# Optimization experiments

Hardware: AMD Instinct MI355X
Metric: run time of the kernel (lower is better)

## Reference

```python
import jax, jax.numpy as jnp
import numpy as np

B, S, E, H = 2, 2048, 1024, 16
D = E // H  # head_dim = 64


def setup_inputs() -> dict:
    key = jax.random.key(0)
    ks = jax.random.split(key, 14)
    inp = {
        "query": jax.random.normal(ks[0], (B, S, E), jnp.float32),
        "key": jax.random.normal(ks[1], (B, S, E), jnp.float32),
        "value": jax.random.normal(ks[2], (B, S, E), jnp.float32),
        "adj": jax.random.normal(ks[3], (S, S), jnp.float32),
        "mask": jax.random.randint(ks[4], (B, 1, S, S), 0, 2, jnp.int32),
    }
    sc = 1.0 / np.sqrt(E)
    inp["Wq"] = jax.random.normal(ks[5], (E, E), jnp.float32) * sc
    inp["bq"] = jax.random.normal(ks[6], (E,), jnp.float32) * sc
    inp["Wk"] = jax.random.normal(ks[7], (E, E), jnp.float32) * sc
    inp["bk"] = jax.random.normal(ks[8], (E,), jnp.float32) * sc
    inp["Wv"] = jax.random.normal(ks[9], (E, E), jnp.float32) * sc
    inp["bv"] = jax.random.normal(ks[10], (E,), jnp.float32) * sc
    inp["Wo"] = jax.random.normal(ks[11], (E, E), jnp.float32) * sc
    inp["bo"] = jax.random.normal(ks[12], (E,), jnp.float32) * sc
    return inp


def reference(query, key, value, adj, mask, Wq, bq, Wk, bk, Wv, bv, Wo, bo):
    b, s, _ = query.shape
    # projections, split into heads: [B,S,E] -> [B,H,S,D]
    def heads(x, W, bias):
        y = jnp.einsum("bse,ef->bsf", x, W.T) + bias
        return y.reshape(b, s, H, D).transpose(0, 2, 1, 3)

    Q = heads(query, Wq, bq)
    K = heads(key, Wk, bk)
    V = heads(value, Wv, bv)

    # scores: [B,H,S,S], scaled by sqrt(head_dim), plus adjacency bias
    scores = jnp.einsum("bhqd,bhkd->bhqk", Q, K) / jnp.sqrt(jnp.float32(D))
    scores = scores + adj[None, None, :, :]
    scores = jnp.where(mask == 0, jnp.float32(-jnp.inf), scores)

    weights = jax.nn.softmax(scores, axis=-1)
    out = jnp.einsum("bhqk,bhkd->bhqd", weights, V)
    out = out.transpose(0, 2, 1, 3).reshape(b, s, E)
    return jnp.einsum("bse,ef->bsf", out, Wo.T) + bo
```

## Files before the change

### kernel.cpp

```cpp
#include <hip/hip_runtime.h>


typedef unsigned short ushort_t;
typedef __attribute__((ext_vector_type(8))) short bf16x8;
typedef __attribute__((ext_vector_type(4))) float floatx4;
typedef __attribute__((ext_vector_type(2))) unsigned int uintx2;

#define NB 2
#define NS 2048
#define NE 1024
#define NH 16
#define ND 64
#define LOG2E 1.44269504f

__device__ __forceinline__ unsigned short f2bf(float f) {
  unsigned int u = __float_as_uint(f);
  return (unsigned short)((u + 0x7fffu + ((u >> 16) & 1u)) >> 16);
}
__device__ __forceinline__ float bf2f(unsigned short h) {
  return __uint_as_float(((unsigned int)h) << 16);
}

__device__ __forceinline__ void gload_lds16(const void* g, void* l) {
  __builtin_amdgcn_global_load_lds(
      (const __attribute__((address_space(1))) unsigned int*)g,
      (__attribute__((address_space(3))) unsigned int*)l, 16, 0, 0);
}

__device__ __forceinline__ uintx2 gload8(const void* p) {
  uintx2 r;
  asm volatile("global_load_dwordx2 %0, %1, off"
               : "=v"(r) : "v"(p) : "memory");
  return r;
}

__device__ __forceinline__ float fexp2(float x) {
#if __has_builtin(__builtin_amdgcn_exp2f)
  return __builtin_amdgcn_exp2f(x);
#else
  return exp2f(x);
#endif
}

__device__ __forceinline__ unsigned int cvtpk_bf16(float lo, float hi) {
  unsigned int r;
  asm("v_cvt_pk_bf16_f32 %0, %1, %2" : "=v"(r) : "v"(lo), "v"(hi));
  return r;
}

__device__ __forceinline__ void pl32swap(unsigned int& a, unsigned int& b) {
#if __has_builtin(__builtin_amdgcn_permlane32_swap)
  uintx2 r = __builtin_amdgcn_permlane32_swap(a, b, false, false);
  a = r[0]; b = r[1];
#else
  asm("v_permlane32_swap_b32 %0, %1" : "+v"(a), "+v"(b));
#endif
}
__device__ __forceinline__ void pl16swap(unsigned int& a, unsigned int& b) {
#if __has_builtin(__builtin_amdgcn_permlane16_swap)
  uintx2 r = __builtin_amdgcn_permlane16_swap(a, b, false, false);
  a = r[0]; b = r[1];
#else
  asm("v_permlane16_swap_b32 %0, %1" : "+v"(a), "+v"(b));
#endif
}

__global__ __launch_bounds__(256) void convert_kernel(
    const float* __restrict__ q, const float* __restrict__ k, const float* __restrict__ v,
    const float* __restrict__ wq, const float* __restrict__ wk,
    const float* __restrict__ wv, const float* __restrict__ wo,
    const float* __restrict__ adj, const int* __restrict__ mask,
    ushort_t* __restrict__ qb, ushort_t* __restrict__ kb, ushort_t* __restrict__ vb,
    ushort_t* __restrict__ wqb, ushort_t* __restrict__ wkb,
    ushort_t* __restrict__ wvb, ushort_t* __restrict__ wob,
    ushort_t* __restrict__ bias)
{
  const long U1 = (long)NB * NS * NE / 8;
  const long U2 = (long)NE * NE / 8;
  long idx = (long)blockIdx.x * 256 + threadIdx.x;
  const float* src;
  ushort_t* dst;
  if (idx < U1) { src = q; dst = qb; }
  else if ((idx -= U1) < U1) { src = k; dst = kb; }
  else if ((idx -= U1) < U1) { src = v; dst = vb; }
  else if ((idx -= U1) < U2) { src = wq; dst = wqb; }
  else if ((idx -= U2) < U2) { src = wk; dst = wkb; }
  else if ((idx -= U2) < U2) { src = wv; dst = wvb; }
  else if ((idx -= U2) < U2) { src = wo; dst = wob; }
  else {
    idx -= U2;
    long flat = idx * 8;
    long rem = flat & ((1L << 22) - 1);
    const float4* a4 = (const float4*)(adj + rem);
    const int4* m4 = (const int4*)(mask + flat);
    float4 a0 = a4[0], a1 = a4[1];
    int4 m0 = m4[0], m1 = m4[1];
    const float NEGV = -1e30f;
    union { ushort_t us[8]; uint4 v4; } o;
    o.us[0] = f2bf((m0.x ? a0.x : NEGV) * LOG2E);
    o.us[1] = f2bf((m0.y ? a0.y : NEGV) * LOG2E);
    o.us[2] = f2bf((m0.z ? a0.z : NEGV) * LOG2E);
    o.us[3] = f2bf((m0.w ? a0.w : NEGV) * LOG2E);
    o.us[4] = f2bf((m1.x ? a1.x : NEGV) * LOG2E);
    o.us[5] = f2bf((m1.y ? a1.y : NEGV) * LOG2E);
    o.us[6] = f2bf((m1.z ? a1.z : NEGV) * LOG2E);
    o.us[7] = f2bf((m1.w ? a1.w : NEGV) * LOG2E);
    ((uint4*)bias)[idx] = o.v4;
    return;
  }
  const float4* s4 = (const float4*)src;
  float4 a0 = s4[idx * 2], a1 = s4[idx * 2 + 1];
  union { ushort_t us[8]; uint4 v4; } o;
  o.us[0] = f2bf(a0.x); o.us[1] = f2bf(a0.y); o.us[2] = f2bf(a0.z); o.us[3] = f2bf(a0.w);
  o.us[4] = f2bf(a1.x); o.us[5] = f2bf(a1.y); o.us[6] = f2bf(a1.z); o.us[7] = f2bf(a1.w);
  ((uint4*)dst)[idx] = o.v4;
}

__global__ __launch_bounds__(256) void qkv_kernel(
    const ushort_t* __restrict__ xq, const ushort_t* __restrict__ xk, const ushort_t* __restrict__ xv,
    const ushort_t* __restrict__ wqb, const ushort_t* __restrict__ wkb, const ushort_t* __restrict__ wvb,
    const float* __restrict__ bq, const float* __restrict__ bk, const float* __restrict__ bvv,
    ushort_t* __restrict__ Qh, ushort_t* __restrict__ Kh, ushort_t* __restrict__ Vt)
{
  __shared__ __align__(16) ushort_t As[3][128 * 32];
  __shared__ __align__(16) ushort_t Bs[3][128 * 32];

  int z = blockIdx.z;
  const ushort_t* X = (z == 0) ? xq : (z == 1) ? xk : xv;
  const ushort_t* W = (z == 0) ? wqb : (z == 1) ? wkb : wvb;
  const float* bias = (z == 0) ? bq : (z == 1) ? bk : bvv;

  int t = threadIdx.x;
  int lane = t & 63, w = t >> 6;
  int quad = lane >> 4, l16 = lane & 15;
  int wr = w >> 1, wc = w & 1;
  int m0 = blockIdx.y * 128, f0 = blockIdx.x * 128;

  int arow = t >> 2, apart = t & 3;
  const ushort_t* Xg = X + (long)(m0 + arow) * NE + apart * 8;
  const ushort_t* Wg = W + (long)(f0 + arow) * NE + apart * 8;

  auto STAGE = [&](int kk, int buf) {
    int k0 = kk * 32;
    gload_lds16(Xg + k0, &As[buf][t * 8]);
    gload_lds16(Xg + k0 + 64 * NE, &As[buf][64 * 32 + t * 8]);
    gload_lds16(Wg + k0, &Bs[buf][t * 8]);
    gload_lds16(Wg + k0 + 64 * NE, &Bs[buf][64 * 32 + t * 8]);
  };
  STAGE(0, 0);
  STAGE(1, 1);

  floatx4 acc[4][4] = {};
  int b = 0;
  for (int k = 0; k < 32; ++k) {
    asm volatile("s_waitcnt vmcnt(4) lgkmcnt(0)" ::: "memory");
    __builtin_amdgcn_s_barrier();
    __builtin_amdgcn_sched_barrier(0);
    int nb = (b == 0) ? 2 : b - 1;
    STAGE((k + 2) & 31, nb);
    const ushort_t* Ab = As[b];
    const ushort_t* Bb = Bs[b];
    bf16x8 af[4], bf[4];
#pragma unroll
    for (int i = 0; i < 4; i++)
      af[i] = *(const bf16x8*)(Ab + (wr * 64 + i * 16 + l16) * 32 + quad * 8);
#pragma unroll
    for (int j = 0; j < 4; j++)
      bf[j] = *(const bf16x8*)(Bb + (wc * 64 + j * 16 + l16) * 32 + quad * 8);
#pragma unroll
    for (int i = 0; i < 4; i++)
#pragma unroll
      for (int j = 0; j < 4; j++)
        acc[i][j] = __builtin_amdgcn_mfma_f32_16x16x32_bf16(af[i], bf[j], acc[i][j], 0, 0, 0);
    b = (b == 2) ? 0 : b + 1;
  }
  asm volatile("s_waitcnt vmcnt(0)" ::: "memory");

  ushort_t* Out = (z == 0) ? Qh : (z == 1) ? Kh : Vt;
  bool isV = (z == 2);
#pragma unroll
  for (int j = 0; j < 4; j++) {
    int f = f0 + wc * 64 + j * 16 + l16;
    float bval = bias[f];
    int h = f >> 6, d = f & 63;
#pragma unroll
    for (int i = 0; i < 4; i++) {
      int mbase = m0 + wr * 64 + i * 16 + quad * 4;
#pragma unroll
      for (int r = 0; r < 4; r++) {
        int m = mbase + r;
        int bb2 = m >> 11, s = m & 2047;
        float y = acc[i][j][r] + bval;
        long off;
        if (!isV) off = ((long)(bb2 * NH + h) * NS + s) * ND + d;
        else      off = ((long)(bb2 * NH + h) * ND + d) * NS + s;
        Out[off] = f2bf(y);
      }
    }
  }
}

__global__ __launch_bounds__(128, 2) void attn_kernel(
    const ushort_t* __restrict__ Qh, const ushort_t* __restrict__ Kh,
    const ushort_t* __restrict__ Vt, const ushort_t* __restrict__ bias,
    ushort_t* __restrict__ aout)
{
  __shared__ __align__(16) ushort_t KVs[2][2][4096];
  __shared__ float Ls[2][64];

  int t = threadIdx.x, lane = t & 63, w = t >> 6;
  int quad = lane >> 4, l16 = lane & 15;
  int orig = blockIdx.x;
  int wg = ((orig & 7) << 7) | (orig >> 3);
  int qt = wg & 31, bh = wg >> 5;
  int bb = bh >> 4, h = bh & 15;
  int q0 = qt * 64;
  int kbase = w * (NS / 2);

  const ushort_t* Qg = Qh + ((long)bh * NS + q0) * ND;
  const ushort_t* Kg = Kh + (long)bh * NS * ND;
  const ushort_t* Vg = Vt + (long)bh * ND * NS;
  const ushort_t* biasg = bias + (long)bb * NS * NS;

  bf16x8 aq[4][2];
#pragma unroll
  for (int m = 0; m < 4; m++)
#pragma unroll
    for (int kd = 0; kd < 2; kd++)
      aq[m][kd] = *(const bf16x8*)(Qg + (long)(m * 16 + l16) * ND + kd * 32 + quad * 8);

  const ushort_t* pK[4];
  const ushort_t* pV[4];
#pragma unroll
  for (int j = 0; j < 4; j++) {
    int ci = j * 64 + lane;
    int row = ci >> 3, cc = (ci & 7) ^ (row & 7);
    pK[j] = Kg + (long)row * ND + cc * 8;
    int sr = ci >> 3, vc2 = (ci & 7) ^ (sr & 7);
    int vrow = sr * 2 + (vc2 >> 2), vpart = vc2 & 3;
    pV[j] = Vg + (long)vrow * NS + vpart * 8;
  }
  const ushort_t* pB[4];
#pragma unroll
  for (int m = 0; m < 4; m++)
    pB[m] = biasg + (long)(q0 + m * 16 + l16) * NS + quad * 4;

  auto STAGE = [&](int tile, int buf) {
    int k0 = kbase + tile * 32;
    ushort_t* Kb = &KVs[w][buf][0];
    ushort_t* Vb = &KVs[w][buf][2048];
#pragma unroll
    for (int j = 0; j < 4; j++)
      gload_lds16(pK[j] + (long)k0 * ND, Kb + (j * 64 + lane) * 8);
#pragma unroll
    for (int j = 0; j < 4; j++)
      gload_lds16(pV[j] + k0, Vb + (j * 64 + lane) * 8);
  };

  uintx2 bc[4][2], bn[4][2];
  auto BLOAD = [&](uintx2 (&dst)[4][2], int tile) {
    int k0 = kbase + tile * 32;
#pragma unroll
    for (int m = 0; m < 4; m++) {
      dst[m][0] = gload8(pB[m] + k0);
      dst[m][1] = gload8(pB[m] + k0 + 16);
    }
  };

  STAGE(0, 0);
  BLOAD(bc, 0);
  STAGE(1, 1);

  floatx4 acc[4][4] = {};
  float lsum[4] = {0.f, 0.f, 0.f, 0.f};
  const int ks_x = l16 & 7;
  const int vs_c = (((l16 & 1) * 4 + quad) ^ (l16 >> 1)) * 8;

#pragma unroll 2
  for (int i = 0; i < 32; ++i) {
    int cur = i & 1;
    const ushort_t* Kb = &KVs[w][cur][0];
    const ushort_t* Vb = &KVs[w][cur][2048];
    asm volatile("s_waitcnt vmcnt(16)" ::: "memory");
    bf16x8 bk[2][2], bv[4];
#pragma unroll
    for (int jk = 0; jk < 2; jk++)
#pragma unroll
      for (int kd = 0; kd < 2; kd++)
        bk[jk][kd] = *(const bf16x8*)(Kb + (jk * 16 + l16) * 64
                                         + ((kd * 4 + quad) ^ ks_x) * 8);
#pragma unroll
    for (int j = 0; j < 4; j++)
      bv[j] = *(const bf16x8*)(Vb + (j * 8 + (l16 >> 1)) * 64 + vs_c);
    asm volatile("s_waitcnt lgkmcnt(0)" ::: "memory");
    BLOAD(bn, (i + 1) & 31);
    STAGE((i + 2) & 31, cur);
    asm volatile("s_waitcnt vmcnt(24)" ::: "memory");
    __builtin_amdgcn_sched_barrier(0);

#pragma unroll
    for (int m = 0; m < 4; m++) {
      floatx4 sc[2] = {};
#pragma unroll
      for (int jk = 0; jk < 2; jk++)
#pragma unroll
        for (int kd = 0; kd < 2; kd++)
          sc[jk] = __builtin_amdgcn_mfma_f32_16x16x32_bf16(bk[jk][kd], aq[m][kd], sc[jk], 0, 0, 0);

      float p[2][4];
#pragma unroll
      for (int jk = 0; jk < 2; jk++) {
        unsigned int d0 = bc[m][jk][0], d1 = bc[m][jk][1];
        float b0 = __uint_as_float(d0 << 16);
        float b1 = __uint_as_float(d0 & 0xffff0000u);
        float b2 = __uint_as_float(d1 << 16);
        float b3 = __uint_as_float(d1 & 0xffff0000u);
        p[jk][0] = fexp2(fmaf(sc[jk][0], 0.125f * LOG2E, b0));
        p[jk][1] = fexp2(fmaf(sc[jk][1], 0.125f * LOG2E, b1));
        p[jk][2] = fexp2(fmaf(sc[jk][2], 0.125f * LOG2E, b2));
        p[jk][3] = fexp2(fmaf(sc[jk][3], 0.125f * LOG2E, b3));
      }
      lsum[m] += ((p[0][0] + p[0][1]) + (p[0][2] + p[0][3]))
               + ((p[1][0] + p[1][1]) + (p[1][2] + p[1][3]));

      unsigned int A0 = cvtpk_bf16(p[0][0], p[0][1]);
      unsigned int A1 = cvtpk_bf16(p[0][2], p[0][3]);
      unsigned int B0 = cvtpk_bf16(p[1][0], p[1][1]);
      unsigned int B1 = cvtpk_bf16(p[1][2], p[1][3]);
      pl32swap(A0, B0); pl16swap(A0, B0);
      pl32swap(A1, B1); pl16swap(A1, B1);
      union { unsigned int u[4]; bf16x8 v8; } pf;
      pf.u[0] = A0; pf.u[1] = A1; pf.u[2] = B0; pf.u[3] = B1;
#pragma unroll
      for (int j = 0; j < 4; j++)
        acc[m][j] = __builtin_amdgcn_mfma_f32_16x16x32_bf16(pf.v8, bv[j], acc[m][j], 0, 0, 0);
    }
#pragma unroll
    for (int m = 0; m < 4; m++) { bc[m][0] = bn[m][0]; bc[m][1] = bn[m][1]; }
  }
  asm volatile("s_waitcnt vmcnt(0)" ::: "memory");

#pragma unroll
  for (int m = 0; m < 4; m++) {
    float s = lsum[m];
    s += __shfl_xor(s, 16);
    s += __shfl_xor(s, 32);
    lsum[m] = s;
  }

  __syncthreads();
  float* C = (float*)&KVs[0][0][0];
  int mo0 = (1 - w) * 2;
#pragma unroll
  for (int mm = 0; mm < 2; mm++) {
    int m = mo0 + mm;
#pragma unroll
    for (int j = 0; j < 4; j++)
      *(floatx4*)(C + (j * 16 + l16) * 64 + (((m * 4 + quad) ^ l16) * 4)) = acc[m][j];
  }
  if (lane < 16) {
    Ls[w][mo0 * 16 + lane]      = lsum[mo0];
    Ls[w][mo0 * 16 + 16 + lane] = lsum[mo0 + 1];
  }
  __syncthreads();

  int ms = w * 2;
  ushort_t* og = aout + (long)bb * NS * NE + h * ND;
#pragma unroll
  for (int mm = 0; mm < 2; mm++) {
    int m = ms + mm;
#pragma unroll
    for (int j = 0; j < 4; j++)
      acc[m][j] += *(const floatx4*)(C + (j * 16 + l16) * 64 + (((m * 4 + quad) ^ l16) * 4));
    float lt = lsum[m] + Ls[1 - w][m * 16 + l16];
#pragma unroll
    for (int r = 0; r < 4; r++) {
      float inv = 1.0f / __shfl(lt, quad * 4 + r);
      int qg = q0 + m * 16 + quad * 4 + r;
#pragma unroll
      for (int j = 0; j < 4; j++)
        og[(long)qg * NE + j * 16 + l16] = f2bf(acc[m][j][r] * inv);
    }
  }
}

__global__ __launch_bounds__(256) void oproj_kernel(
    const ushort_t* __restrict__ A, const ushort_t* __restrict__ Wob,
    const float* __restrict__ bo, float* __restrict__ out)
{
  __shared__ __align__(16) ushort_t As[3][128 * 32];
  __shared__ __align__(16) ushort_t Bs[3][64 * 32];

  int t = threadIdx.x;
  int lane = t & 63, w = t >> 6;
  int quad = lane >> 4, l16 = lane & 15;
  int wr = w >> 1, wc = w & 1;
  int m0 = blockIdx.y * 128, f0 = blockIdx.x * 64;

  int arow = t >> 2, apart = t & 3;
  const ushort_t* Xg = A + (long)(m0 + arow) * NE + apart * 8;
  const ushort_t* Wg = Wob + (long)(f0 + arow) * NE + apart * 8;

  auto STAGE = [&](int kk, int buf) {
    int k0 = kk * 32;
    gload_lds16(Xg + k0, &As[buf][t * 8]);
    gload_lds16(Xg + k0 + 64 * NE, &As[buf][64 * 32 + t * 8]);
    gload_lds16(Wg + k0, &Bs[buf][t * 8]);
  };
  STAGE(0, 0);
  STAGE(1, 1);

  floatx4 acc[4][2] = {};
  int b = 0;
  for (int k = 0; k < 32; ++k) {
    asm volatile("s_waitcnt vmcnt(3) lgkmcnt(0)" ::: "memory");
    __builtin_amdgcn_s_barrier();
    __builtin_amdgcn_sched_barrier(0);
    int nb = (b == 0) ? 2 : b - 1;
    STAGE((k + 2) & 31, nb);
    const ushort_t* Ab = As[b];
    const ushort_t* Bb = Bs[b];
    bf16x8 af[4], bf[2];
#pragma unroll
    for (int i = 0; i < 4; i++)
      af[i] = *(const bf16x8*)(Ab + (wr * 64 + i * 16 + l16) * 32 + quad * 8);
#pragma unroll
    for (int j = 0; j < 2; j++)
      bf[j] = *(const bf16x8*)(Bb + (wc * 32 + j * 16 + l16) * 32 + quad * 8);
#pragma unroll
    for (int i = 0; i < 4; i++)
#pragma unroll
      for (int j = 0; j < 2; j++)
        acc[i][j] = __builtin_amdgcn_mfma_f32_16x16x32_bf16(af[i], bf[j], acc[i][j], 0, 0, 0);
    b = (b == 2) ? 0 : b + 1;
  }
  asm volatile("s_waitcnt vmcnt(0)" ::: "memory");

#pragma unroll
  for (int j = 0; j < 2; j++) {
    int f = f0 + wc * 32 + j * 16 + l16;
    float bval = bo[f];
#pragma unroll
    for (int i = 0; i < 4; i++) {
      int mbase = m0 + wr * 64 + i * 16 + quad * 4;
#pragma unroll
      for (int r = 0; r < 4; r++) {
        int m = mbase + r;
        out[(long)m * NE + f] = acc[i][j][r] + bval;
      }
    }
  }
}

extern "C" void kernel_launch(void* const* d_in, const int* in_sizes, int n_in,
                              void* d_out, int out_size, void* d_ws, size_t ws_size,
                              hipStream_t stream) {
  const float* query = (const float*)d_in[0];
  const float* key   = (const float*)d_in[1];
  const float* value = (const float*)d_in[2];
  const float* adj   = (const float*)d_in[3];
  const int*   mask  = (const int*)d_in[4];
  const float* Wq = (const float*)d_in[5];
  const float* bq = (const float*)d_in[6];
  const float* Wk = (const float*)d_in[7];
  const float* bk = (const float*)d_in[8];
  const float* Wv = (const float*)d_in[9];
  const float* bv = (const float*)d_in[10];
  const float* Wo = (const float*)d_in[11];
  const float* bo = (const float*)d_in[12];
  float* out = (float*)d_out;

  char* ws = (char*)d_ws;
  const size_t MB = 1ull << 20;
  ushort_t* qb   = (ushort_t*)(ws + 0 * MB);
  ushort_t* kb   = (ushort_t*)(ws + 8 * MB);
  ushort_t* vb   = (ushort_t*)(ws + 16 * MB);
  ushort_t* wqb  = (ushort_t*)(ws + 24 * MB);
  ushort_t* wkb  = (ushort_t*)(ws + 26 * MB);
  ushort_t* wvb  = (ushort_t*)(ws + 28 * MB);
  ushort_t* wob  = (ushort_t*)(ws + 30 * MB);
  ushort_t* Qh   = (ushort_t*)(ws + 32 * MB);
  ushort_t* Kh   = (ushort_t*)(ws + 40 * MB);
  ushort_t* Vt   = (ushort_t*)(ws + 48 * MB);
  ushort_t* aout = (ushort_t*)(ws + 56 * MB);
  ushort_t* bias = (ushort_t*)(ws + 64 * MB);

  convert_kernel<<<12288, 256, 0, stream>>>(query, key, value, Wq, Wk, Wv, Wo,
                                            adj, mask, qb, kb, vb, wqb, wkb, wvb, wob, bias);
  qkv_kernel<<<dim3(8, 32, 3), 256, 0, stream>>>(qb, kb, vb, wqb, wkb, wvb,
                                                 bq, bk, bv, Qh, Kh, Vt);
  attn_kernel<<<dim3(1024), 128, 0, stream>>>(Qh, Kh, Vt, bias, aout);
  oproj_kernel<<<dim3(16, 32), 256, 0, stream>>>(aout, wob, bo, out);
}
```

Measured before the change: 328.7 us.

## Split attention keys across blocks with shared 4-stage LDS ring and combine kernel

Restructures the attention kernel so each 256-thread block covers 128 query rows over half the key range. All four waves share one K/V tile staged into a 4-deep LDS ring with block barriers, where before each wave streamed its own copy. Each key half writes bf16 normalized partial outputs and row sums to workspace, and a new combine kernel merges them with sum weights and writes the head-interleaved layout. This cuts redundant K/V staging per query and raises occupancy, at the cost of extra global traffic for the partials and an extra launch.

```diff
diff --git a/kernel.cpp b/kernel.cpp
--- a/kernel.cpp
+++ b/kernel.cpp
@@ -200,88 +200,63 @@
   }
 }
 
-__global__ __launch_bounds__(128, 2) void attn_kernel(
+__global__ __launch_bounds__(256, 3) void attn_kernel(
     const ushort_t* __restrict__ Qh, const ushort_t* __restrict__ Kh,
     const ushort_t* __restrict__ Vt, const ushort_t* __restrict__ bias,
-    ushort_t* __restrict__ aout)
+    ushort_t* __restrict__ PO, float* __restrict__ L)
 {
-  __shared__ __align__(16) ushort_t KVs[2][2][4096];
-  __shared__ float Ls[2][64];
+  __shared__ __align__(16) ushort_t KVs[4][4096];
 
   int t = threadIdx.x, lane = t & 63, w = t >> 6;
   int quad = lane >> 4, l16 = lane & 15;
   int orig = blockIdx.x;
   int wg = ((orig & 7) << 7) | (orig >> 3);
-  int qt = wg & 31, bh = wg >> 5;
-  int bb = bh >> 4, h = bh & 15;
-  int q0 = qt * 64;
-  int kbase = w * (NS / 2);
+  int bh = wg >> 5, qt = (wg >> 1) & 15, ks = wg & 1;
+  int q0 = qt * 128;
+  int kbase = ks * (NS / 2);
 
   const ushort_t* Qg = Qh + ((long)bh * NS + q0) * ND;
-  const ushort_t* Kg = Kh + (long)bh * NS * ND;
-  const ushort_t* Vg = Vt + (long)bh * ND * NS;
-  const ushort_t* biasg = bias + (long)bb * NS * NS;
-
-  bf16x8 aq[4][2];
-#pragma unroll
-  for (int m = 0; m < 4; m++)
+  const ushort_t* Kg = Kh + ((long)bh * NS + kbase) * ND;
+  const ushort_t* Vg = Vt + (long)bh * ND * NS + kbase;
+  const ushort_t* biasg = bias + (long)(bh >> 4) * NS * NS;
+
+  bf16x8 aq[2][2];
+#pragma unroll
+  for (int m = 0; m < 2; m++)
 #pragma unroll
     for (int kd = 0; kd < 2; kd++)
-      aq[m][kd] = *(const bf16x8*)(Qg + (long)(m * 16 + l16) * ND + kd * 32 + quad * 8);
-
-  const ushort_t* pK[4];
-  const ushort_t* pV[4];
-#pragma unroll
-  for (int j = 0; j < 4; j++) {
-    int ci = j * 64 + lane;
-    int row = ci >> 3, cc = (ci & 7) ^ (row & 7);
-    pK[j] = Kg + (long)row * ND + cc * 8;
-    int sr = ci >> 3, vc2 = (ci & 7) ^ (sr & 7);
-    int vrow = sr * 2 + (vc2 >> 2), vpart = vc2 & 3;
-    pV[j] = Vg + (long)vrow * NS + vpart * 8;
-  }
-  const ushort_t* pB[4];
-#pragma unroll
-  for (int m = 0; m < 4; m++)
-    pB[m] = biasg + (long)(q0 + m * 16 + l16) * NS + quad * 4;
+      aq[m][kd] = *(const bf16x8*)(Qg + (long)(w * 32 + m * 16 + l16) * ND
+                                      + kd * 32 + quad * 8);
+
+  int krow = t >> 3, kc = (t & 7) ^ (krow & 7);
+  int vsr = t >> 3, vc2 = (t & 7) ^ (vsr & 7);
+  int vrow = vsr * 2 + (vc2 >> 2), vpart = vc2 & 3;
+  const ushort_t* Kgp = Kg + (long)krow * ND + kc * 8;
+  const ushort_t* Vgp = Vg + (long)vrow * NS + vpart * 8;
+  const ushort_t* pB0 = biasg + (long)(q0 + w * 32 + l16) * NS + kbase + quad * 4;
+  const ushort_t* pB1 = pB0 + 16 * NS;
 
   auto STAGE = [&](int tile, int buf) {
-    int k0 = kbase + tile * 32;
-    ushort_t* Kb = &KVs[w][buf][0];
-    ushort_t* Vb = &KVs[w][buf][2048];
-#pragma unroll
-    for (int j = 0; j < 4; j++)
-      gload_lds16(pK[j] + (long)k0 * ND, Kb + (j * 64 + lane) * 8);
-#pragma unroll
-    for (int j = 0; j < 4; j++)
-      gload_lds16(pV[j] + k0, Vb + (j * 64 + lane) * 8);
+    int k0 = tile * 32;
+    gload_lds16(Kgp + (long)k0 * ND, &KVs[buf][t * 8]);
+    gload_lds16(Vgp + k0, &KVs[buf][2048 + t * 8]);
   };
-
-  uintx2 bc[4][2], bn[4][2];
-  auto BLOAD = [&](uintx2 (&dst)[4][2], int tile) {
-    int k0 = kbase + tile * 32;
-#pragma unroll
-    for (int m = 0; m < 4; m++) {
-      dst[m][0] = gload8(pB[m] + k0);
-      dst[m][1] = gload8(pB[m] + k0 + 16);
-    }
+  uintx2 bcA[2][2], bcB[2][2];
+  auto BLOAD = [&](uintx2 (&dst)[2][2], int tile) {
+    long off = (long)tile * 32;
+    dst[0][0] = gload8(pB0 + off);
+    dst[0][1] = gload8(pB0 + off + 16);
+    dst[1][0] = gload8(pB1 + off);
+    dst[1][1] = gload8(pB1 + off + 16);
   };
 
-  STAGE(0, 0);
-  BLOAD(bc, 0);
-  STAGE(1, 1);
-
-  floatx4 acc[4][4] = {};
-  float lsum[4] = {0.f, 0.f, 0.f, 0.f};
+  floatx4 acc[2][4] = {};
+  float lsum[2] = {0.f, 0.f};
   const int ks_x = l16 & 7;
   const int vs_c = (((l16 & 1) * 4 + quad) ^ (l16 >> 1)) * 8;
 
-#pragma unroll 2
-  for (int i = 0; i < 32; ++i) {
-    int cur = i & 1;
-    const ushort_t* Kb = &KVs[w][cur][0];
-    const ushort_t* Vb = &KVs[w][cur][2048];
-    asm volatile("s_waitcnt vmcnt(16)" ::: "memory");
+  auto BODY = [&](const ushort_t* Kb, const ushort_t* Vb,
+                  const uintx2 (&bcv)[2][2]) {
     bf16x8 bk[2][2], bv[4];
 #pragma unroll
     for (int jk = 0; jk < 2; jk++)
@@ -292,25 +267,18 @@
 #pragma unroll
     for (int j = 0; j < 4; j++)
       bv[j] = *(const bf16x8*)(Vb + (j * 8 + (l16 >> 1)) * 64 + vs_c);
-    asm volatile("s_waitcnt lgkmcnt(0)" ::: "memory");
-    BLOAD(bn, (i + 1) & 31);
-    STAGE((i + 2) & 31, cur);
-    asm volatile("s_waitcnt vmcnt(24)" ::: "memory");
-    __builtin_amdgcn_sched_barrier(0);
-
-#pragma unroll
-    for (int m = 0; m < 4; m++) {
+#pragma unroll
+    for (int m = 0; m < 2; m++) {
       floatx4 sc[2] = {};
 #pragma unroll
       for (int jk = 0; jk < 2; jk++)
 #pragma unroll
         for (int kd = 0; kd < 2; kd++)
           sc[jk] = __builtin_amdgcn_mfma_f32_16x16x32_bf16(bk[jk][kd], aq[m][kd], sc[jk], 0, 0, 0);
-
       float p[2][4];
 #pragma unroll
       for (int jk = 0; jk < 2; jk++) {
-        unsigned int d0 = bc[m][jk][0], d1 = bc[m][jk][1];
+        unsigned int d0 = bcv[m][jk][0], d1 = bcv[m][jk][1];
         float b0 = __uint_as_float(d0 << 16);
         float b1 = __uint_as_float(d0 & 0xffff0000u);
         float b2 = __uint_as_float(d1 << 16);
@@ -322,7 +290,6 @@
       }
       lsum[m] += ((p[0][0] + p[0][1]) + (p[0][2] + p[0][3]))
                + ((p[1][0] + p[1][1]) + (p[1][2] + p[1][3]));
-
       unsigned int A0 = cvtpk_bf16(p[0][0], p[0][1]);
       unsigned int A1 = cvtpk_bf16(p[0][2], p[0][3]);
       unsigned int B0 = cvtpk_bf16(p[1][0], p[1][1]);
@@ -335,53 +302,91 @@
       for (int j = 0; j < 4; j++)
         acc[m][j] = __builtin_amdgcn_mfma_f32_16x16x32_bf16(pf.v8, bv[j], acc[m][j], 0, 0, 0);
     }
-#pragma unroll
-    for (int m = 0; m < 4; m++) { bc[m][0] = bn[m][0]; bc[m][1] = bn[m][1]; }
-  }
+  };
+
+#define SB() __builtin_amdgcn_sched_barrier(0)
+#define WAIT2()                                                   \
+  asm volatile("s_waitcnt vmcnt(2) lgkmcnt(0)" ::: "memory");     \
+  __builtin_amdgcn_s_barrier();                                   \
+  SB()
+
+  SB();
   asm volatile("s_waitcnt vmcnt(0)" ::: "memory");
-
-#pragma unroll
-  for (int m = 0; m < 4; m++) {
+  SB();
+  STAGE(0, 0); SB();
+  BLOAD(bcA, 0); SB();
+  STAGE(1, 1); SB();
+
+#pragma unroll 1
+  for (int ii = 0; ii < 7; ++ii) {
+    int base = ii * 4;
+    WAIT2(); BLOAD(bcB, base + 1); SB(); STAGE(base + 2, 2); SB();
+    BODY(&KVs[0][0], &KVs[0][2048], bcA);
+    WAIT2(); BLOAD(bcA, base + 2); SB(); STAGE(base + 3, 3); SB();
+    BODY(&KVs[1][0], &KVs[1][2048], bcB);
+    WAIT2(); BLOAD(bcB, base + 3); SB(); STAGE(base + 4, 0); SB();
+    BODY(&KVs[2][0], &KVs[2][2048], bcA);
+    WAIT2(); BLOAD(bcA, base + 4); SB(); STAGE(base + 5, 1); SB();
+    BODY(&KVs[3][0], &KVs[3][2048], bcB);
+  }
+  WAIT2(); BLOAD(bcB, 29); SB(); STAGE(30, 2); SB();
+  BODY(&KVs[0][0], &KVs[0][2048], bcA);
+  WAIT2(); BLOAD(bcA, 30); SB(); STAGE(31, 3); SB();
+  BODY(&KVs[1][0], &KVs[1][2048], bcB);
+  WAIT2(); BLOAD(bcB, 31); SB();
+  BODY(&KVs[2][0], &KVs[2][2048], bcA);
+  asm volatile("s_waitcnt vmcnt(0) lgkmcnt(0)" ::: "memory");
+  __builtin_amdgcn_s_barrier();
+  SB();
+  BODY(&KVs[3][0], &KVs[3][2048], bcB);
+
+#undef WAIT2
+#undef SB
+
+#pragma unroll
+  for (int m = 0; m < 2; m++) {
     float s = lsum[m];
     s += __shfl_xor(s, 16);
     s += __shfl_xor(s, 32);
     lsum[m] = s;
   }
 
-  __syncthreads();
-  float* C = (float*)&KVs[0][0][0];
-  int mo0 = (1 - w) * 2;
-#pragma unroll
-  for (int mm = 0; mm < 2; mm++) {
-    int m = mo0 + mm;
-#pragma unroll
-    for (int j = 0; j < 4; j++)
-      *(floatx4*)(C + (j * 16 + l16) * 64 + (((m * 4 + quad) ^ l16) * 4)) = acc[m][j];
-  }
-  if (lane < 16) {
-    Ls[w][mo0 * 16 + lane]      = lsum[mo0];
-    Ls[w][mo0 * 16 + 16 + lane] = lsum[mo0 + 1];
-  }
-  __syncthreads();
-
-  int ms = w * 2;
-  ushort_t* og = aout + (long)bb * NS * NE + h * ND;
-#pragma unroll
-  for (int mm = 0; mm < 2; mm++) {
-    int m = ms + mm;
-#pragma unroll
-    for (int j = 0; j < 4; j++)
-      acc[m][j] += *(const floatx4*)(C + (j * 16 + l16) * 64 + (((m * 4 + quad) ^ l16) * 4));
-    float lt = lsum[m] + Ls[1 - w][m * 16 + l16];
+  ushort_t* pog = PO + (long)ks * 4194304 + (long)bh * 131072 + qt * 8192;
+  float* Lg = L + ks * 65536 + bh * 2048 + qt * 128;
+#pragma unroll
+  for (int m = 0; m < 2; m++) {
 #pragma unroll
     for (int r = 0; r < 4; r++) {
-      float inv = 1.0f / __shfl(lt, quad * 4 + r);
-      int qg = q0 + m * 16 + quad * 4 + r;
+      float inv = 1.0f / __shfl(lsum[m], quad * 4 + r);
+      int row = w * 32 + m * 16 + quad * 4 + r;
 #pragma unroll
       for (int j = 0; j < 4; j++)
-        og[(long)qg * NE + j * 16 + l16] = f2bf(acc[m][j][r] * inv);
+        pog[row * 64 + j * 16 + l16] = f2bf(acc[m][j][r] * inv);
     }
-  }
+    if (quad == 0) Lg[w * 32 + m * 16 + l16] = lsum[m];
+  }
+}
+
+__global__ __launch_bounds__(256) void combine_kernel(
+    const ushort_t* __restrict__ PO, const float* __restrict__ L,
+    ushort_t* __restrict__ aout)
+{
+  int idx = blockIdx.x * 256 + threadIdx.x;
+  long f = (long)idx * 8;
+  int r = (int)(f >> 6);
+  float l0 = L[r], l1 = L[65536 + r];
+  float inv = 1.0f / (l0 + l1);
+  float w0 = l0 * inv, w1 = l1 * inv;
+  union { uint4 v4; ushort_t us[8]; } ua, ub, o;
+  ua.v4 = ((const uint4*)PO)[idx];
+  ub.v4 = ((const uint4*)(PO + 4194304))[idx];
+#pragma unroll
+  for (int j = 0; j < 8; j++)
+    o.us[j] = f2bf(w0 * bf2f(ua.us[j]) + w1 * bf2f(ub.us[j]));
+  int q = r & 127, qt = (r >> 7) & 15, bh = r >> 11;
+  int b_ = bh >> 4, h = bh & 15, d0 = (int)(f & 63);
+  long off = (long)(b_ * NS + qt * 128 + q) * NE + h * ND + d0;
+  *(uint4*)(aout + off) = o.v4;
 }
 
 __global__ __launch_bounds__(256) void oproj_kernel(
@@ -484,11 +489,14 @@
   ushort_t* Vt   = (ushort_t*)(ws + 48 * MB);
   ushort_t* aout = (ushort_t*)(ws + 56 * MB);
   ushort_t* bias = (ushort_t*)(ws + 64 * MB);
+  ushort_t* PO   = (ushort_t*)(ws + 0 * MB);
+  float*    Lp   = (float*)(ws + 16 * MB);
 
   convert_kernel<<<12288, 256, 0, stream>>>(query, key, value, Wq, Wk, Wv, Wo,
                                             adj, mask, qb, kb, vb, wqb, wkb, wvb, wob, bias);
   qkv_kernel<<<dim3(8, 32, 3), 256, 0, stream>>>(qb, kb, vb, wqb, wkb, wvb,
                                                  bq, bk, bv, Qh, Kh, Vt);
-  attn_kernel<<<dim3(1024), 128, 0, stream>>>(Qh, Kh, Vt, bias, aout);
+  attn_kernel<<<dim3(1024), 256, 0, stream>>>(Qh, Kh, Vt, bias, PO, Lp);
+  combine_kernel<<<dim3(2048), 256, 0, stream>>>(PO, Lp, aout);
   oproj_kernel<<<dim3(16, 32), 256, 0, stream>>>(aout, wob, bo, out);
 }
```

Measured after the change: 319.3 us. 1.03x faster.
